# Optimization experiments

Hardware: AMD Instinct MI355X
Metric: run time of the kernel (lower is better)

## Reference

```python
import jax, jax.numpy as jnp
import numpy as np
from jax import lax

B, S, H = 2, 1024, 1024
I = 512            # moe_intermediate_size
E = 32             # n_routed_experts
TOP_K = 4
N_GROUP = 4
TOPK_GROUP = 2
SCALE = 2.5        # routed_scaling_factor
N_SHARED = 2
SH_I = I * N_SHARED


def setup_inputs() -> dict:
    key = jax.random.key(0)
    ks = jax.random.split(key, 10)
    std = 0.02
    return {
        "hidden_states": jax.random.normal(ks[0], (B, S, H), jnp.float32),
        "router_weight": jax.random.normal(ks[1], (E, H), jnp.float32) * std,
        "router_bias": jnp.zeros((E,), jnp.float32),
        "gate_w": jax.random.normal(ks[2], (E, I, H), jnp.float32) * std,
        "up_w": jax.random.normal(ks[3], (E, I, H), jnp.float32) * std,
        "down_w": jax.random.normal(ks[4], (E, H, I), jnp.float32) * std,
        "shared_gate_w": jax.random.normal(ks[5], (SH_I, H), jnp.float32) * std,
        "shared_up_w": jax.random.normal(ks[6], (SH_I, H), jnp.float32) * std,
        "shared_down_w": jax.random.normal(ks[7], (H, SH_I), jnp.float32) * std,
    }


def _route(tokens, router_weight, router_bias):
    # tokens: [T, H] -> topk_idx [T, K] int, topk_weight [T, K] f32
    logits = tokens.astype(jnp.float32) @ router_weight.astype(jnp.float32).T  # [T, E]
    scores = jax.nn.sigmoid(logits)
    sfc = scores + router_bias[None, :]
    T = tokens.shape[0]
    # group scores: sum of top-2 per group
    grp = sfc.reshape(T, N_GROUP, E // N_GROUP)
    group_scores = lax.top_k(grp, 2)[0].sum(-1)                 # [T, n_group]
    _, gidx = lax.top_k(group_scores, TOPK_GROUP)               # [T, topk_group]
    gmask = jax.nn.one_hot(gidx, N_GROUP, dtype=sfc.dtype).sum(1)  # [T, n_group]
    smask = jnp.broadcast_to(gmask[:, :, None], (T, N_GROUP, E // N_GROUP)).reshape(T, E)
    tmp = jnp.where(smask > 0, sfc, 0.0)
    _, topk_idx = lax.top_k(tmp, TOP_K)                         # [T, K]
    topk_w = jnp.take_along_axis(scores, topk_idx, axis=1)
    topk_w = topk_w / (topk_w.sum(-1, keepdims=True) + 1e-20)   # norm_topk_prob
    topk_w = topk_w * SCALE
    return topk_idx, topk_w


def reference(hidden_states, router_weight, router_bias, gate_w, up_w, down_w,
              shared_gate_w, shared_up_w, shared_down_w):
    tokens = hidden_states.reshape(-1, H)                       # [T, H]
    topk_idx, topk_w = _route(tokens, router_weight, router_bias)
    # dense all-expert SwiGLU
    gate_vals = jax.nn.silu(jnp.einsum('th,eih->tei', tokens, gate_w))
    up_vals = jnp.einsum('th,eih->tei', tokens, up_w)
    hidden_vals = gate_vals * up_vals                           # [T, E, I]
    expert_out = jnp.einsum('tei,ehi->teh', hidden_vals, down_w)  # [T, E, H]
    sel = jnp.take_along_axis(expert_out, topk_idx[:, :, None], axis=1)  # [T, K, H]
    mixed = (sel * topk_w[:, :, None].astype(sel.dtype)).sum(1)
    mixed = mixed.reshape(hidden_states.shape)
    # shared experts (dense SwiGLU MLP)
    sg = jax.nn.silu(jnp.einsum('bsh,ih->bsi', hidden_states, shared_gate_w))
    su = jnp.einsum('bsh,ih->bsi', hidden_states, shared_up_w)
    shared = jnp.einsum('bsi,hi->bsh', sg * su, shared_down_w)
    return mixed + shared
```

## Files before the change

### kernel.cpp

```cpp
#include <hip/hip_runtime.h>
#include <hip/hip_bf16.h>
#include <math.h>

#define HD 1024
#define ID 512
#define NE 32
#define NT 2048
#define NG 4
#define SHI 1024
#define SCALE 2.5f

#define BM 128
#define BN 64
#define BK 32
#define LDA 40

typedef __bf16 bf16_t;
typedef __attribute__((ext_vector_type(8))) __bf16 bf16x8;
typedef __attribute__((ext_vector_type(4))) __bf16 bf16x4;
typedef __attribute__((ext_vector_type(4))) float f32x4;

#define LTOK 8
#define LKC 64
__global__ void __launch_bounds__(256) logits_kernel(
    const float* __restrict__ hs, const float* __restrict__ rw,
    float* __restrict__ logits, int* __restrict__ counts)
{
    if (blockIdx.x == 0 && threadIdx.x < NE) counts[threadIdx.x] = 0;

    __shared__ float Xs[LTOK][68];
    __shared__ float Ws[NE][65];

    int tid = threadIdx.x;
    int t0 = blockIdx.x * LTOK;
    int tslot = tid >> 5, ecol = tid & 31;
    float acc = 0.f;

    for (int k0 = 0; k0 < HD; k0 += LKC) {
        if (tid < 128) {
            int row = tid >> 4, q = tid & 15;
            float4 v = *(const float4*)(hs + (size_t)(t0 + row) * HD + k0 + q * 4);
            *(float4*)(&Xs[row][q * 4]) = v;
        }
        #pragma unroll
        for (int i = 0; i < 8; ++i) {
            int idx = i * 256 + tid;
            int e = idx >> 6, kk = idx & 63;
            Ws[e][kk] = rw[(size_t)e * HD + k0 + kk];
        }
        __syncthreads();
        #pragma unroll 8
        for (int kk = 0; kk < LKC; ++kk)
            acc += Xs[tslot][kk] * Ws[ecol][kk];
        __syncthreads();
    }
    logits[(size_t)(t0 + tslot) * NE + ecol] = acc;
}

__global__ void __launch_bounds__(256) topk_kernel(
    const float* __restrict__ logits, const float* __restrict__ rb,
    float* __restrict__ topkw, int* __restrict__ counts, int* __restrict__ lists)
{
    int t = blockIdx.x * 256 + threadIdx.x;
    if (t >= NT) return;

    float scores[NE], sfc[NE], tmp[NE];
    #pragma unroll
    for (int e = 0; e < NE; ++e) {
        float l = logits[(size_t)t * NE + e];
        float s = 1.f / (1.f + __expf(-l));
        scores[e] = s;
        sfc[e] = s + rb[e];
    }
    float gs[NG];
    #pragma unroll
    for (int g = 0; g < NG; ++g) {
        float m1 = -1e30f, m2 = -1e30f;
        #pragma unroll
        for (int j = 0; j < 8; ++j) {
            float v = sfc[g * 8 + j];
            if (v > m1) { m2 = m1; m1 = v; } else if (v > m2) m2 = v;
        }
        gs[g] = m1 + m2;
    }
    int g1 = 0;
    #pragma unroll
    for (int g = 1; g < NG; ++g) if (gs[g] > gs[g1]) g1 = g;
    int g2 = -1;
    #pragma unroll
    for (int g = 0; g < NG; ++g) {
        if (g == g1) continue;
        if (g2 < 0 || gs[g] > gs[g2]) g2 = g;
    }
    #pragma unroll
    for (int e = 0; e < NE; ++e) {
        int g = e >> 3;
        tmp[e] = (g == g1 || g == g2) ? sfc[e] : 0.0f;
    }
    int idx[4]; float wk[4]; float wsum = 0.f;
    #pragma unroll
    for (int k = 0; k < 4; ++k) {
        int best = 0; float bv = -1e30f;
        #pragma unroll
        for (int e = 0; e < NE; ++e) if (tmp[e] > bv) { bv = tmp[e]; best = e; }
        idx[k] = best; tmp[best] = -1e30f;
        wk[k] = scores[best]; wsum += wk[k];
    }
    float inv = SCALE / (wsum + 1e-20f);
    #pragma unroll
    for (int k = 0; k < 4; ++k) {
        int p = t * 4 + k;
        topkw[p] = wk[k] * inv;
        int e = idx[k];
        int pos = atomicAdd(&counts[e], 1);
        lists[e * NT + pos] = p;
    }
}

__device__ inline bf16x4 cvt4(float4 v) {
    bf16x4 r;
    r[0] = (__bf16)v.x; r[1] = (__bf16)v.y; r[2] = (__bf16)v.z; r[3] = (__bf16)v.w;
    return r;
}

template<bool EXPERT, int ND>
__global__ void __launch_bounds__(256) gateup_mfma(
    const float* __restrict__ X, const float* __restrict__ Wg,
    const float* __restrict__ Wu, bf16_t* __restrict__ Hout,
    const int* __restrict__ lists, const int* __restrict__ counts)
{
    int e = 0, cnt = NT;
    const float* wg = Wg; const float* wu = Wu;
    if (EXPERT) {
        e = blockIdx.x; cnt = counts[e];
        wg = Wg + (size_t)e * ND * HD;
        wu = Wu + (size_t)e * ND * HD;
    }
    int mtb = blockIdx.y, ntb = blockIdx.z;
    if (mtb * BM >= cnt) return;

    __shared__ __align__(16) bf16_t As[BM * LDA];
    __shared__ __align__(16) bf16_t Bgs[BN * LDA];
    __shared__ __align__(16) bf16_t Bus[BN * LDA];
    __shared__ int rowid[BM];

    int tid = threadIdx.x;
    if (tid < BM) {
        int gm = mtb * BM + tid;
        int mm = gm < cnt ? gm : cnt - 1;
        rowid[tid] = EXPERT ? lists[e * NT + mm] : mm;
    }
    __syncthreads();

    int lane = tid & 63;
    int w = tid >> 6;
    int wm = w & 1, wn = w >> 1;
    int lrow = lane & 15, quad = lane >> 4;

    f32x4 accg[4][2], accu[4][2];
    #pragma unroll
    for (int i = 0; i < 4; ++i)
        #pragma unroll
        for (int j = 0; j < 2; ++j) { accg[i][j] = (f32x4){0,0,0,0}; accu[i][j] = (f32x4){0,0,0,0}; }

    for (int k0 = 0; k0 < HD; k0 += BK) {
        #pragma unroll
        for (int r = 0; r < (BM * (BK / 4)) / 256; ++r) {
            int idx = r * 256 + tid;
            int row = idx >> 3, kq = idx & 7;
            int tok = EXPERT ? (rowid[row] >> 2) : rowid[row];
            float4 v = *(const float4*)(X + (size_t)tok * HD + k0 + kq * 4);
            *(bf16x4*)(As + row * LDA + kq * 4) = cvt4(v);
        }
        #pragma unroll
        for (int r = 0; r < (BN * (BK / 4)) / 256; ++r) {
            int idx = r * 256 + tid;
            int n = idx >> 3, kq = idx & 7;
            size_t off = (size_t)(ntb * BN + n) * HD + k0 + kq * 4;
            *(bf16x4*)(Bgs + n * LDA + kq * 4) = cvt4(*(const float4*)(wg + off));
            *(bf16x4*)(Bus + n * LDA + kq * 4) = cvt4(*(const float4*)(wu + off));
        }
        __syncthreads();

        bf16x8 af[4], bg[2], bu[2];
        #pragma unroll
        for (int mt = 0; mt < 4; ++mt)
            af[mt] = *(const bf16x8*)(As + (wm * 64 + mt * 16 + lrow) * LDA + quad * 8);
        #pragma unroll
        for (int nt = 0; nt < 2; ++nt) {
            bg[nt] = *(const bf16x8*)(Bgs + (wn * 32 + nt * 16 + lrow) * LDA + quad * 8);
            bu[nt] = *(const bf16x8*)(Bus + (wn * 32 + nt * 16 + lrow) * LDA + quad * 8);
        }
        #pragma unroll
        for (int mt = 0; mt < 4; ++mt)
            #pragma unroll
            for (int nt = 0; nt < 2; ++nt) {
                accg[mt][nt] = __builtin_amdgcn_mfma_f32_16x16x32_bf16(af[mt], bg[nt], accg[mt][nt], 0, 0, 0);
                accu[mt][nt] = __builtin_amdgcn_mfma_f32_16x16x32_bf16(af[mt], bu[nt], accu[mt][nt], 0, 0, 0);
            }
        __syncthreads();
    }

    #pragma unroll
    for (int mt = 0; mt < 4; ++mt)
        #pragma unroll
        for (int r = 0; r < 4; ++r) {
            int row_local = wm * 64 + mt * 16 + quad * 4 + r;
            int gm = mtb * BM + row_local;
            if (gm >= cnt) continue;
            int p = rowid[row_local];
            #pragma unroll
            for (int nt = 0; nt < 2; ++nt) {
                int col = ntb * BN + wn * 32 + nt * 16 + lrow;
                float g = accg[mt][nt][r], u = accu[mt][nt][r];
                float h = (g / (1.f + __expf(-g))) * u;
                Hout[(size_t)p * ND + col] = (__bf16)h;
            }
        }
}

template<bool EXPERT, int KD>
__global__ void __launch_bounds__(256) down_mfma(
    const bf16_t* __restrict__ Hin, const float* __restrict__ Wd,
    float* __restrict__ out, const int* __restrict__ lists,
    const int* __restrict__ counts, const float* __restrict__ topkw)
{
    int e = 0, cnt = NT;
    const float* wd = Wd;
    if (EXPERT) {
        e = blockIdx.x; cnt = counts[e];
        wd = Wd + (size_t)e * HD * KD;
    }
    int mtb = blockIdx.y, ntb = blockIdx.z;
    if (mtb * BM >= cnt) return;

    __shared__ __align__(16) bf16_t As[BM * LDA];
    __shared__ __align__(16) bf16_t Ws[BN * LDA];
    __shared__ int rowid[BM];

    int tid = threadIdx.x;
    if (tid < BM) {
        int gm = mtb * BM + tid;
        int mm = gm < cnt ? gm : cnt - 1;
        rowid[tid] = EXPERT ? lists[e * NT + mm] : mm;
    }
    __syncthreads();

    int lane = tid & 63;
    int w = tid >> 6;
    int wm = w & 1, wn = w >> 1;
    int lrow = lane & 15, quad = lane >> 4;

    f32x4 acc[4][2];
    #pragma unroll
    for (int i = 0; i < 4; ++i)
        #pragma unroll
        for (int j = 0; j < 2; ++j) acc[i][j] = (f32x4){0,0,0,0};

    for (int k0 = 0; k0 < KD; k0 += BK) {
        #pragma unroll
        for (int r = 0; r < (BM * (BK / 8)) / 256; ++r) {
            int idx = r * 256 + tid;
            int row = idx >> 2, c = idx & 3;
            int rp = rowid[row];
            bf16x8 v = *(const bf16x8*)(Hin + (size_t)rp * KD + k0 + c * 8);
            *(bf16x8*)(As + row * LDA + c * 8) = v;
        }
        #pragma unroll
        for (int r = 0; r < (BN * (BK / 4)) / 256; ++r) {
            int idx = r * 256 + tid;
            int n = idx >> 3, kq = idx & 7;
            size_t off = (size_t)(ntb * BN + n) * KD + k0 + kq * 4;
            *(bf16x4*)(Ws + n * LDA + kq * 4) = cvt4(*(const float4*)(wd + off));
        }
        __syncthreads();

        bf16x8 af[4], bf[2];
        #pragma unroll
        for (int mt = 0; mt < 4; ++mt)
            af[mt] = *(const bf16x8*)(As + (wm * 64 + mt * 16 + lrow) * LDA + quad * 8);
        #pragma unroll
        for (int nt = 0; nt < 2; ++nt)
            bf[nt] = *(const bf16x8*)(Ws + (wn * 32 + nt * 16 + lrow) * LDA + quad * 8);
        #pragma unroll
        for (int mt = 0; mt < 4; ++mt)
            #pragma unroll
            for (int nt = 0; nt < 2; ++nt)
                acc[mt][nt] = __builtin_amdgcn_mfma_f32_16x16x32_bf16(af[mt], bf[nt], acc[mt][nt], 0, 0, 0);
        __syncthreads();
    }

    #pragma unroll
    for (int mt = 0; mt < 4; ++mt)
        #pragma unroll
        for (int r = 0; r < 4; ++r) {
            int row_local = wm * 64 + mt * 16 + quad * 4 + r;
            int gm = mtb * BM + row_local;
            if (gm >= cnt) continue;
            int p = rowid[row_local];
            #pragma unroll
            for (int nt = 0; nt < 2; ++nt) {
                int col = ntb * BN + wn * 32 + nt * 16 + lrow;
                float val = acc[mt][nt][r];
                if (EXPERT) {
                    float wgt = topkw[p];
                    atomicAdd(&out[(size_t)(p >> 2) * HD + col], wgt * val);
                } else {
                    out[(size_t)p * HD + col] = val;
                }
            }
        }
}

extern "C" void kernel_launch(void* const* d_in, const int* in_sizes, int n_in,
                              void* d_out, int out_size, void* d_ws, size_t ws_size,
                              hipStream_t stream) {
    const float* hs  = (const float*)d_in[0];
    const float* rw  = (const float*)d_in[1];
    const float* rb  = (const float*)d_in[2];
    const float* gw  = (const float*)d_in[3];
    const float* uw  = (const float*)d_in[4];
    const float* dw  = (const float*)d_in[5];
    const float* sgw = (const float*)d_in[6];
    const float* suw = (const float*)d_in[7];
    const float* sdw = (const float*)d_in[8];
    float* out = (float*)d_out;

    char* ws = (char*)d_ws;
    int*    counts = (int*)ws;
    float*  topkw  = (float*)(ws + 128);
    int*    lists  = (int*)(ws + 128 + 32768);
    float*  logits = (float*)(ws + 128 + 32768 + 262144);
    bf16_t* hbuf   = (bf16_t*)(ws + 128 + 32768 + 262144 + 262144);

    logits_kernel<<<NT / LTOK, 256, 0, stream>>>(hs, rw, logits, counts);
    topk_kernel<<<NT / 256, 256, 0, stream>>>(logits, rb, topkw, counts, lists);

    gateup_mfma<false, SHI><<<dim3(1, NT / BM, SHI / BN), 256, 0, stream>>>(
        hs, sgw, suw, hbuf, nullptr, nullptr);
    down_mfma<false, SHI><<<dim3(1, NT / BM, HD / BN), 256, 0, stream>>>(
        hbuf, sdw, out, nullptr, nullptr, nullptr);

    gateup_mfma<true, ID><<<dim3(NE, NT / BM, ID / BN), 256, 0, stream>>>(
        hs, gw, uw, hbuf, lists, counts);
    down_mfma<true, ID><<<dim3(NE, NT / BM, HD / BN), 256, 0, stream>>>(
        hbuf, dw, out, lists, counts, topkw);
}
```

Before: 418.4 us.

## Prefetch next K-tile into registers and shrink shared-expert M tile

The gate/up and down MFMA kernels now load the next K-slice of activations and weights into registers while the current slice is being multiplied. This overlaps global load latency with compute. The M tile becomes a template parameter, set to 64 for the dense shared-expert GEMMs to launch more blocks and to 128 for the routed experts. The cost is more live registers per thread, which may lower occupancy.

```diff
diff --git a/kernel.cpp b/kernel.cpp
--- a/kernel.cpp
+++ b/kernel.cpp
@@ -10,7 +10,6 @@
 #define SHI 1024
 #define SCALE 2.5f
 
-#define BM 128
 #define BN 64
 #define BK 32
 #define LDA 40
@@ -123,7 +122,7 @@
     return r;
 }
 
-template<bool EXPERT, int ND>
+template<bool EXPERT, int ND, int BMT>
 __global__ void __launch_bounds__(256) gateup_mfma(
     const float* __restrict__ X, const float* __restrict__ Wg,
     const float* __restrict__ Wu, bf16_t* __restrict__ Hout,
@@ -137,62 +136,100 @@
         wu = Wu + (size_t)e * ND * HD;
     }
     int mtb = blockIdx.y, ntb = blockIdx.z;
-    if (mtb * BM >= cnt) return;
-
-    __shared__ __align__(16) bf16_t As[BM * LDA];
+    if (mtb * BMT >= cnt) return;
+
+    __shared__ __align__(16) bf16_t As[BMT * LDA];
     __shared__ __align__(16) bf16_t Bgs[BN * LDA];
     __shared__ __align__(16) bf16_t Bus[BN * LDA];
-    __shared__ int rowid[BM];
+    __shared__ int rowid[BMT];
 
     int tid = threadIdx.x;
-    if (tid < BM) {
-        int gm = mtb * BM + tid;
+    if (tid < BMT) {
+        int gm = mtb * BMT + tid;
         int mm = gm < cnt ? gm : cnt - 1;
         rowid[tid] = EXPERT ? lists[e * NT + mm] : mm;
     }
     __syncthreads();
+
+    constexpr int AR = (BMT * BK) / (256 * 4);
+    constexpr int BR = (BN * BK) / (256 * 4);
+    constexpr int MT = BMT / 32;
 
     int lane = tid & 63;
     int w = tid >> 6;
     int wm = w & 1, wn = w >> 1;
     int lrow = lane & 15, quad = lane >> 4;
 
-    f32x4 accg[4][2], accu[4][2];
-    #pragma unroll
-    for (int i = 0; i < 4; ++i)
+    f32x4 accg[MT][2], accu[MT][2];
+    #pragma unroll
+    for (int i = 0; i < MT; ++i)
         #pragma unroll
         for (int j = 0; j < 2; ++j) { accg[i][j] = (f32x4){0,0,0,0}; accu[i][j] = (f32x4){0,0,0,0}; }
 
+    float4 pa[AR], pbg[BR], pbu[BR];
+
+    #pragma unroll
+    for (int r = 0; r < AR; ++r) {
+        int idx = r * 256 + tid;
+        int row = idx >> 3, kq = idx & 7;
+        int tok = EXPERT ? (rowid[row] >> 2) : rowid[row];
+        pa[r] = *(const float4*)(X + (size_t)tok * HD + kq * 4);
+    }
+    #pragma unroll
+    for (int r = 0; r < BR; ++r) {
+        int idx = r * 256 + tid;
+        int n = idx >> 3, kq = idx & 7;
+        size_t off = (size_t)(ntb * BN + n) * HD + kq * 4;
+        pbg[r] = *(const float4*)(wg + off);
+        pbu[r] = *(const float4*)(wu + off);
+    }
+
     for (int k0 = 0; k0 < HD; k0 += BK) {
         #pragma unroll
-        for (int r = 0; r < (BM * (BK / 4)) / 256; ++r) {
+        for (int r = 0; r < AR; ++r) {
             int idx = r * 256 + tid;
             int row = idx >> 3, kq = idx & 7;
-            int tok = EXPERT ? (rowid[row] >> 2) : rowid[row];
-            float4 v = *(const float4*)(X + (size_t)tok * HD + k0 + kq * 4);
-            *(bf16x4*)(As + row * LDA + kq * 4) = cvt4(v);
-        }
-        #pragma unroll
-        for (int r = 0; r < (BN * (BK / 4)) / 256; ++r) {
+            *(bf16x4*)(As + row * LDA + kq * 4) = cvt4(pa[r]);
+        }
+        #pragma unroll
+        for (int r = 0; r < BR; ++r) {
             int idx = r * 256 + tid;
             int n = idx >> 3, kq = idx & 7;
-            size_t off = (size_t)(ntb * BN + n) * HD + k0 + kq * 4;
-            *(bf16x4*)(Bgs + n * LDA + kq * 4) = cvt4(*(const float4*)(wg + off));
-            *(bf16x4*)(Bus + n * LDA + kq * 4) = cvt4(*(const float4*)(wu + off));
-        }
-        __syncthreads();
-
-        bf16x8 af[4], bg[2], bu[2];
-        #pragma unroll
-        for (int mt = 0; mt < 4; ++mt)
-            af[mt] = *(const bf16x8*)(As + (wm * 64 + mt * 16 + lrow) * LDA + quad * 8);
+            *(bf16x4*)(Bgs + n * LDA + kq * 4) = cvt4(pbg[r]);
+            *(bf16x4*)(Bus + n * LDA + kq * 4) = cvt4(pbu[r]);
+        }
+        __syncthreads();
+
+        int k1 = k0 + BK;
+        if (k1 < HD) {
+            #pragma unroll
+            for (int r = 0; r < AR; ++r) {
+                int idx = r * 256 + tid;
+                int row = idx >> 3, kq = idx & 7;
+                int tok = EXPERT ? (rowid[row] >> 2) : rowid[row];
+                pa[r] = *(const float4*)(X + (size_t)tok * HD + k1 + kq * 4);
+            }
+            #pragma unroll
+            for (int r = 0; r < BR; ++r) {
+                int idx = r * 256 + tid;
+                int n = idx >> 3, kq = idx & 7;
+                size_t off = (size_t)(ntb * BN + n) * HD + k1 + kq * 4;
+                pbg[r] = *(const float4*)(wg + off);
+                pbu[r] = *(const float4*)(wu + off);
+            }
+        }
+
+        bf16x8 af[MT], bg[2], bu[2];
+        #pragma unroll
+        for (int mt = 0; mt < MT; ++mt)
+            af[mt] = *(const bf16x8*)(As + (wm * (BMT / 2) + mt * 16 + lrow) * LDA + quad * 8);
         #pragma unroll
         for (int nt = 0; nt < 2; ++nt) {
             bg[nt] = *(const bf16x8*)(Bgs + (wn * 32 + nt * 16 + lrow) * LDA + quad * 8);
             bu[nt] = *(const bf16x8*)(Bus + (wn * 32 + nt * 16 + lrow) * LDA + quad * 8);
         }
         #pragma unroll
-        for (int mt = 0; mt < 4; ++mt)
+        for (int mt = 0; mt < MT; ++mt)
             #pragma unroll
             for (int nt = 0; nt < 2; ++nt) {
                 accg[mt][nt] = __builtin_amdgcn_mfma_f32_16x16x32_bf16(af[mt], bg[nt], accg[mt][nt], 0, 0, 0);
@@ -202,11 +239,11 @@
     }
 
     #pragma unroll
-    for (int mt = 0; mt < 4; ++mt)
+    for (int mt = 0; mt < MT; ++mt)
         #pragma unroll
         for (int r = 0; r < 4; ++r) {
-            int row_local = wm * 64 + mt * 16 + quad * 4 + r;
-            int gm = mtb * BM + row_local;
+            int row_local = wm * (BMT / 2) + mt * 16 + quad * 4 + r;
+            int gm = mtb * BMT + row_local;
             if (gm >= cnt) continue;
             int p = rowid[row_local];
             #pragma unroll
@@ -219,7 +256,7 @@
         }
 }
 
-template<bool EXPERT, int KD>
+template<bool EXPERT, int KD, int BMT>
 __global__ void __launch_bounds__(256) down_mfma(
     const bf16_t* __restrict__ Hin, const float* __restrict__ Wd,
     float* __restrict__ out, const int* __restrict__ lists,
@@ -232,58 +269,91 @@
         wd = Wd + (size_t)e * HD * KD;
     }
     int mtb = blockIdx.y, ntb = blockIdx.z;
-    if (mtb * BM >= cnt) return;
-
-    __shared__ __align__(16) bf16_t As[BM * LDA];
+    if (mtb * BMT >= cnt) return;
+
+    __shared__ __align__(16) bf16_t As[BMT * LDA];
     __shared__ __align__(16) bf16_t Ws[BN * LDA];
-    __shared__ int rowid[BM];
+    __shared__ int rowid[BMT];
 
     int tid = threadIdx.x;
-    if (tid < BM) {
-        int gm = mtb * BM + tid;
+    if (tid < BMT) {
+        int gm = mtb * BMT + tid;
         int mm = gm < cnt ? gm : cnt - 1;
         rowid[tid] = EXPERT ? lists[e * NT + mm] : mm;
     }
     __syncthreads();
+
+    constexpr int ARH = (BMT * BK / 8) / 256;
+    constexpr int BR = (BN * BK) / (256 * 4);
+    constexpr int MT = BMT / 32;
 
     int lane = tid & 63;
     int w = tid >> 6;
     int wm = w & 1, wn = w >> 1;
     int lrow = lane & 15, quad = lane >> 4;
 
-    f32x4 acc[4][2];
-    #pragma unroll
-    for (int i = 0; i < 4; ++i)
+    f32x4 acc[MT][2];
+    #pragma unroll
+    for (int i = 0; i < MT; ++i)
         #pragma unroll
         for (int j = 0; j < 2; ++j) acc[i][j] = (f32x4){0,0,0,0};
 
+    bf16x8 pa[ARH];
+    float4 pw[BR];
+
+    #pragma unroll
+    for (int r = 0; r < ARH; ++r) {
+        int idx = r * 256 + tid;
+        int row = idx >> 2, c = idx & 3;
+        pa[r] = *(const bf16x8*)(Hin + (size_t)rowid[row] * KD + c * 8);
+    }
+    #pragma unroll
+    for (int r = 0; r < BR; ++r) {
+        int idx = r * 256 + tid;
+        int n = idx >> 3, kq = idx & 7;
+        pw[r] = *(const float4*)(wd + (size_t)(ntb * BN + n) * KD + kq * 4);
+    }
+
     for (int k0 = 0; k0 < KD; k0 += BK) {
         #pragma unroll
-        for (int r = 0; r < (BM * (BK / 8)) / 256; ++r) {
+        for (int r = 0; r < ARH; ++r) {
             int idx = r * 256 + tid;
             int row = idx >> 2, c = idx & 3;
-            int rp = rowid[row];
-            bf16x8 v = *(const bf16x8*)(Hin + (size_t)rp * KD + k0 + c * 8);
-            *(bf16x8*)(As + row * LDA + c * 8) = v;
-        }
-        #pragma unroll
-        for (int r = 0; r < (BN * (BK / 4)) / 256; ++r) {
+            *(bf16x8*)(As + row * LDA + c * 8) = pa[r];
+        }
+        #pragma unroll
+        for (int r = 0; r < BR; ++r) {
             int idx = r * 256 + tid;
             int n = idx >> 3, kq = idx & 7;
-            size_t off = (size_t)(ntb * BN + n) * KD + k0 + kq * 4;
-            *(bf16x4*)(Ws + n * LDA + kq * 4) = cvt4(*(const float4*)(wd + off));
-        }
-        __syncthreads();
-
-        bf16x8 af[4], bf[2];
-        #pragma unroll
-        for (int mt = 0; mt < 4; ++mt)
-            af[mt] = *(const bf16x8*)(As + (wm * 64 + mt * 16 + lrow) * LDA + quad * 8);
+            *(bf16x4*)(Ws + n * LDA + kq * 4) = cvt4(pw[r]);
+        }
+        __syncthreads();
+
+        int k1 = k0 + BK;
+        if (k1 < KD) {
+            #pragma unroll
+            for (int r = 0; r < ARH; ++r) {
+                int idx = r * 256 + tid;
+                int row = idx >> 2, c = idx & 3;
+                pa[r] = *(const bf16x8*)(Hin + (size_t)rowid[row] * KD + k1 + c * 8);
+            }
+            #pragma unroll
+            for (int r = 0; r < BR; ++r) {
+                int idx = r * 256 + tid;
+                int n = idx >> 3, kq = idx & 7;
+                pw[r] = *(const float4*)(wd + (size_t)(ntb * BN + n) * KD + k1 + kq * 4);
+            }
+        }
+
+        bf16x8 af[MT], bf[2];
+        #pragma unroll
+        for (int mt = 0; mt < MT; ++mt)
+            af[mt] = *(const bf16x8*)(As + (wm * (BMT / 2) + mt * 16 + lrow) * LDA + quad * 8);
         #pragma unroll
         for (int nt = 0; nt < 2; ++nt)
             bf[nt] = *(const bf16x8*)(Ws + (wn * 32 + nt * 16 + lrow) * LDA + quad * 8);
         #pragma unroll
-        for (int mt = 0; mt < 4; ++mt)
+        for (int mt = 0; mt < MT; ++mt)
             #pragma unroll
             for (int nt = 0; nt < 2; ++nt)
                 acc[mt][nt] = __builtin_amdgcn_mfma_f32_16x16x32_bf16(af[mt], bf[nt], acc[mt][nt], 0, 0, 0);
@@ -291,11 +361,11 @@
     }
 
     #pragma unroll
-    for (int mt = 0; mt < 4; ++mt)
+    for (int mt = 0; mt < MT; ++mt)
         #pragma unroll
         for (int r = 0; r < 4; ++r) {
-            int row_local = wm * 64 + mt * 16 + quad * 4 + r;
-            int gm = mtb * BM + row_local;
+            int row_local = wm * (BMT / 2) + mt * 16 + quad * 4 + r;
+            int gm = mtb * BMT + row_local;
             if (gm >= cnt) continue;
             int p = rowid[row_local];
             #pragma unroll
@@ -336,13 +406,13 @@
     logits_kernel<<<NT / LTOK, 256, 0, stream>>>(hs, rw, logits, counts);
     topk_kernel<<<NT / 256, 256, 0, stream>>>(logits, rb, topkw, counts, lists);
 
-    gateup_mfma<false, SHI><<<dim3(1, NT / BM, SHI / BN), 256, 0, stream>>>(
+    gateup_mfma<false, SHI, 64><<<dim3(1, NT / 64, SHI / BN), 256, 0, stream>>>(
         hs, sgw, suw, hbuf, nullptr, nullptr);
-    down_mfma<false, SHI><<<dim3(1, NT / BM, HD / BN), 256, 0, stream>>>(
+    down_mfma<false, SHI, 64><<<dim3(1, NT / 64, HD / BN), 256, 0, stream>>>(
         hbuf, sdw, out, nullptr, nullptr, nullptr);
 
-    gateup_mfma<true, ID><<<dim3(NE, NT / BM, ID / BN), 256, 0, stream>>>(
+    gateup_mfma<true, ID, 128><<<dim3(NE, NT / 128, ID / BN), 256, 0, stream>>>(
         hs, gw, uw, hbuf, lists, counts);
-    down_mfma<true, ID><<<dim3(NE, NT / BM, HD / BN), 256, 0, stream>>>(
+    down_mfma<true, ID, 128><<<dim3(NE, NT / 128, HD / BN), 256, 0, stream>>>(
         hbuf, dw, out, lists, counts, topkw);
 }
```

New measurement: 411.6 us. About the same (-1.6%).

## Pre-convert inputs and weights to bf16, stage tiles via global_load_lds

Applied to the files above, without the earlier changes.

Adds a conversion pass that writes bf16 copies of hidden states and all expert and shared weights into the workspace. New GEMM kernels then load tiles straight into LDS with global_load_lds, dropping per-tile fp32 loads and register-side conversion. The old fp32 path is kept as a fallback when the workspace is too small. The trade-off is an extra full read and write of every weight on each call (about 200MB of fp32 read), plus unpadded LDS layouts that may cause bank conflicts.

```diff
diff --git a/kernel.cpp b/kernel.cpp
--- a/kernel.cpp
+++ b/kernel.cpp
@@ -10,15 +10,33 @@
 #define SHI 1024
 #define SCALE 2.5f
 
-#define BM 128
-#define BN 64
 #define BK 32
-#define LDA 40
+#define LDAF 40
 
 typedef __bf16 bf16_t;
 typedef __attribute__((ext_vector_type(8))) __bf16 bf16x8;
 typedef __attribute__((ext_vector_type(4))) __bf16 bf16x4;
 typedef __attribute__((ext_vector_type(4))) float f32x4;
+
+__device__ inline void load_lds16(const void* g, void* l) {
+    __builtin_amdgcn_global_load_lds(
+        (const __attribute__((address_space(1))) void*)g,
+        (__attribute__((address_space(3))) void*)l, 16, 0, 0);
+}
+
+__global__ void __launch_bounds__(256) cvt_bf16_kernel(
+    const float* __restrict__ in, bf16_t* __restrict__ out, int n8)
+{
+    int stride = gridDim.x * 256;
+    for (int i = blockIdx.x * 256 + threadIdx.x; i < n8; i += stride) {
+        const float4* p = (const float4*)(in + (size_t)i * 8);
+        float4 a = p[0], b = p[1];
+        bf16x8 v;
+        v[0] = (__bf16)a.x; v[1] = (__bf16)a.y; v[2] = (__bf16)a.z; v[3] = (__bf16)a.w;
+        v[4] = (__bf16)b.x; v[5] = (__bf16)b.y; v[6] = (__bf16)b.z; v[7] = (__bf16)b.w;
+        *(bf16x8*)(out + (size_t)i * 8) = v;
+    }
+}
 
 #define LTOK 8
 #define LKC 64
@@ -123,8 +141,200 @@
     return r;
 }
 
+
 template<bool EXPERT, int ND>
-__global__ void __launch_bounds__(256) gateup_mfma(
+__global__ void __launch_bounds__(256) gateup_bf16(
+    const bf16_t* __restrict__ X, const bf16_t* __restrict__ Wg,
+    const bf16_t* __restrict__ Wu, bf16_t* __restrict__ Hout,
+    const int* __restrict__ lists, const int* __restrict__ counts)
+{
+    int e = 0, cnt = NT;
+    const bf16_t* wg = Wg; const bf16_t* wu = Wu;
+    if (EXPERT) {
+        e = blockIdx.x; cnt = counts[e];
+        wg = Wg + (size_t)e * ND * HD;
+        wu = Wu + (size_t)e * ND * HD;
+    }
+    int mtb = blockIdx.y, ntb = blockIdx.z;
+    if (mtb * 128 >= cnt) return;
+
+    __shared__ __align__(16) bf16_t As[128 * 32];
+    __shared__ __align__(16) bf16_t Bgs[64 * 32];
+    __shared__ __align__(16) bf16_t Bus[64 * 32];
+    __shared__ int rowid[128];
+
+    int tid = threadIdx.x;
+    if (tid < 128) {
+        int gm = mtb * 128 + tid;
+        int mm = gm < cnt ? gm : cnt - 1;
+        rowid[tid] = EXPERT ? lists[e * NT + mm] : mm;
+    }
+    __syncthreads();
+
+    int lane = tid & 63, w = tid >> 6;
+    int wm = w & 1, wn = w >> 1;
+    int lrow = lane & 15, quad = lane >> 4;
+
+    int sr = lane >> 2, sc = lane & 3;
+    int arow0 = w * 32 + sr;
+    int arow1 = w * 32 + 16 + sr;
+    int tokA0 = EXPERT ? (rowid[arow0] >> 2) : rowid[arow0];
+    int tokA1 = EXPERT ? (rowid[arow1] >> 2) : rowid[arow1];
+    const bf16_t* ga0 = X + (size_t)tokA0 * HD + sc * 8;
+    const bf16_t* ga1 = X + (size_t)tokA1 * HD + sc * 8;
+    bf16_t* la0 = As + (w * 32) * 32 + lane * 8;
+    bf16_t* la1 = As + (w * 32 + 16) * 32 + lane * 8;
+
+    int brow = w * 16 + sr;
+    const bf16_t* gbg = wg + (size_t)(ntb * 64 + brow) * HD + sc * 8;
+    const bf16_t* gbu = wu + (size_t)(ntb * 64 + brow) * HD + sc * 8;
+    bf16_t* lbg = Bgs + (w * 16) * 32 + lane * 8;
+    bf16_t* lbu = Bus + (w * 16) * 32 + lane * 8;
+
+    f32x4 accg[4][2], accu[4][2];
+    #pragma unroll
+    for (int i = 0; i < 4; ++i)
+        #pragma unroll
+        for (int j = 0; j < 2; ++j) { accg[i][j] = (f32x4){0,0,0,0}; accu[i][j] = (f32x4){0,0,0,0}; }
+
+    for (int k0 = 0; k0 < HD; k0 += BK) {
+        load_lds16(ga0 + k0, la0);
+        load_lds16(ga1 + k0, la1);
+        load_lds16(gbg + k0, lbg);
+        load_lds16(gbu + k0, lbu);
+        __syncthreads();
+
+        bf16x8 af[4], bg[2], bu[2];
+        #pragma unroll
+        for (int mt = 0; mt < 4; ++mt)
+            af[mt] = *(const bf16x8*)(As + (wm * 64 + mt * 16 + lrow) * 32 + quad * 8);
+        #pragma unroll
+        for (int nt = 0; nt < 2; ++nt) {
+            bg[nt] = *(const bf16x8*)(Bgs + (wn * 32 + nt * 16 + lrow) * 32 + quad * 8);
+            bu[nt] = *(const bf16x8*)(Bus + (wn * 32 + nt * 16 + lrow) * 32 + quad * 8);
+        }
+        #pragma unroll
+        for (int mt = 0; mt < 4; ++mt)
+            #pragma unroll
+            for (int nt = 0; nt < 2; ++nt) {
+                accg[mt][nt] = __builtin_amdgcn_mfma_f32_16x16x32_bf16(af[mt], bg[nt], accg[mt][nt], 0, 0, 0);
+                accu[mt][nt] = __builtin_amdgcn_mfma_f32_16x16x32_bf16(af[mt], bu[nt], accu[mt][nt], 0, 0, 0);
+            }
+        __syncthreads();
+    }
+
+    #pragma unroll
+    for (int mt = 0; mt < 4; ++mt)
+        #pragma unroll
+        for (int r = 0; r < 4; ++r) {
+            int row_local = wm * 64 + mt * 16 + quad * 4 + r;
+            int gm = mtb * 128 + row_local;
+            if (gm >= cnt) continue;
+            int p = rowid[row_local];
+            #pragma unroll
+            for (int nt = 0; nt < 2; ++nt) {
+                int col = ntb * 64 + wn * 32 + nt * 16 + lrow;
+                float g = accg[mt][nt][r], u = accu[mt][nt][r];
+                float h = (g / (1.f + __expf(-g))) * u;
+                Hout[(size_t)p * ND + col] = (__bf16)h;
+            }
+        }
+}
+
+template<bool EXPERT, int KD>
+__global__ void __launch_bounds__(256) down_bf16(
+    const bf16_t* __restrict__ Hin, const bf16_t* __restrict__ Wd,
+    float* __restrict__ out, const int* __restrict__ lists,
+    const int* __restrict__ counts, const float* __restrict__ topkw)
+{
+    int e = 0, cnt = NT;
+    const bf16_t* wd = Wd;
+    if (EXPERT) {
+        e = blockIdx.x; cnt = counts[e];
+        wd = Wd + (size_t)e * HD * KD;
+    }
+    int mtb = blockIdx.y, ntb = blockIdx.z;
+    if (mtb * 128 >= cnt) return;
+
+    __shared__ __align__(16) bf16_t As[128 * 32];
+    __shared__ __align__(16) bf16_t Bs[64 * 32];
+    __shared__ int rowid[128];
+
+    int tid = threadIdx.x;
+    if (tid < 128) {
+        int gm = mtb * 128 + tid;
+        int mm = gm < cnt ? gm : cnt - 1;
+        rowid[tid] = EXPERT ? lists[e * NT + mm] : mm;
+    }
+    __syncthreads();
+
+    int lane = tid & 63, w = tid >> 6;
+    int wm = w & 1, wn = w >> 1;
+    int lrow = lane & 15, quad = lane >> 4;
+
+    int sr = lane >> 2, sc = lane & 3;
+    int arow0 = w * 32 + sr;
+    int arow1 = w * 32 + 16 + sr;
+    const bf16_t* ga0 = Hin + (size_t)rowid[arow0] * KD + sc * 8;
+    const bf16_t* ga1 = Hin + (size_t)rowid[arow1] * KD + sc * 8;
+    bf16_t* la0 = As + (w * 32) * 32 + lane * 8;
+    bf16_t* la1 = As + (w * 32 + 16) * 32 + lane * 8;
+
+    int brow = w * 16 + sr;
+    const bf16_t* gb = wd + (size_t)(ntb * 64 + brow) * KD + sc * 8;
+    bf16_t* lb = Bs + (w * 16) * 32 + lane * 8;
+
+    f32x4 acc[4][2];
+    #pragma unroll
+    for (int i = 0; i < 4; ++i)
+        #pragma unroll
+        for (int j = 0; j < 2; ++j) acc[i][j] = (f32x4){0,0,0,0};
+
+    for (int k0 = 0; k0 < KD; k0 += BK) {
+        load_lds16(ga0 + k0, la0);
+        load_lds16(ga1 + k0, la1);
+        load_lds16(gb + k0, lb);
+        __syncthreads();
+
+        bf16x8 af[4], bf[2];
+        #pragma unroll
+        for (int mt = 0; mt < 4; ++mt)
+            af[mt] = *(const bf16x8*)(As + (wm * 64 + mt * 16 + lrow) * 32 + quad * 8);
+        #pragma unroll
+        for (int nt = 0; nt < 2; ++nt)
+            bf[nt] = *(const bf16x8*)(Bs + (wn * 32 + nt * 16 + lrow) * 32 + quad * 8);
+        #pragma unroll
+        for (int mt = 0; mt < 4; ++mt)
+            #pragma unroll
+            for (int nt = 0; nt < 2; ++nt)
+                acc[mt][nt] = __builtin_amdgcn_mfma_f32_16x16x32_bf16(af[mt], bf[nt], acc[mt][nt], 0, 0, 0);
+        __syncthreads();
+    }
+
+    #pragma unroll
+    for (int mt = 0; mt < 4; ++mt)
+        #pragma unroll
+        for (int r = 0; r < 4; ++r) {
+            int row_local = wm * 64 + mt * 16 + quad * 4 + r;
+            int gm = mtb * 128 + row_local;
+            if (gm >= cnt) continue;
+            int p = rowid[row_local];
+            #pragma unroll
+            for (int nt = 0; nt < 2; ++nt) {
+                int col = ntb * 64 + wn * 32 + nt * 16 + lrow;
+                float val = acc[mt][nt][r];
+                if (EXPERT) {
+                    float wgt = topkw[p];
+                    atomicAdd(&out[(size_t)(p >> 2) * HD + col], wgt * val);
+                } else {
+                    out[(size_t)p * HD + col] = val;
+                }
+            }
+        }
+}
+
+template<bool EXPERT, int ND>
+__global__ void __launch_bounds__(256) gateup_f32(
     const float* __restrict__ X, const float* __restrict__ Wg,
     const float* __restrict__ Wu, bf16_t* __restrict__ Hout,
     const int* __restrict__ lists, const int* __restrict__ counts)
@@ -137,23 +347,22 @@
         wu = Wu + (size_t)e * ND * HD;
     }
     int mtb = blockIdx.y, ntb = blockIdx.z;
-    if (mtb * BM >= cnt) return;
-
-    __shared__ __align__(16) bf16_t As[BM * LDA];
-    __shared__ __align__(16) bf16_t Bgs[BN * LDA];
-    __shared__ __align__(16) bf16_t Bus[BN * LDA];
-    __shared__ int rowid[BM];
+    if (mtb * 128 >= cnt) return;
+
+    __shared__ __align__(16) bf16_t As[128 * LDAF];
+    __shared__ __align__(16) bf16_t Bgs[64 * LDAF];
+    __shared__ __align__(16) bf16_t Bus[64 * LDAF];
+    __shared__ int rowid[128];
 
     int tid = threadIdx.x;
-    if (tid < BM) {
-        int gm = mtb * BM + tid;
+    if (tid < 128) {
+        int gm = mtb * 128 + tid;
         int mm = gm < cnt ? gm : cnt - 1;
         rowid[tid] = EXPERT ? lists[e * NT + mm] : mm;
     }
     __syncthreads();
 
-    int lane = tid & 63;
-    int w = tid >> 6;
+    int lane = tid & 63, w = tid >> 6;
     int wm = w & 1, wn = w >> 1;
     int lrow = lane & 15, quad = lane >> 4;
 
@@ -165,31 +374,31 @@
 
     for (int k0 = 0; k0 < HD; k0 += BK) {
         #pragma unroll
-        for (int r = 0; r < (BM * (BK / 4)) / 256; ++r) {
+        for (int r = 0; r < 4; ++r) {
             int idx = r * 256 + tid;
             int row = idx >> 3, kq = idx & 7;
             int tok = EXPERT ? (rowid[row] >> 2) : rowid[row];
             float4 v = *(const float4*)(X + (size_t)tok * HD + k0 + kq * 4);
-            *(bf16x4*)(As + row * LDA + kq * 4) = cvt4(v);
-        }
-        #pragma unroll
-        for (int r = 0; r < (BN * (BK / 4)) / 256; ++r) {
+            *(bf16x4*)(As + row * LDAF + kq * 4) = cvt4(v);
+        }
+        #pragma unroll
+        for (int r = 0; r < 2; ++r) {
             int idx = r * 256 + tid;
             int n = idx >> 3, kq = idx & 7;
-            size_t off = (size_t)(ntb * BN + n) * HD + k0 + kq * 4;
-            *(bf16x4*)(Bgs + n * LDA + kq * 4) = cvt4(*(const float4*)(wg + off));
-            *(bf16x4*)(Bus + n * LDA + kq * 4) = cvt4(*(const float4*)(wu + off));
+            size_t off = (size_t)(ntb * 64 + n) * HD + k0 + kq * 4;
+            *(bf16x4*)(Bgs + n * LDAF + kq * 4) = cvt4(*(const float4*)(wg + off));
+            *(bf16x4*)(Bus + n * LDAF + kq * 4) = cvt4(*(const float4*)(wu + off));
         }
         __syncthreads();
 
         bf16x8 af[4], bg[2], bu[2];
         #pragma unroll
         for (int mt = 0; mt < 4; ++mt)
-            af[mt] = *(const bf16x8*)(As + (wm * 64 + mt * 16 + lrow) * LDA + quad * 8);
+            af[mt] = *(const bf16x8*)(As + (wm * 64 + mt * 16 + lrow) * LDAF + quad * 8);
         #pragma unroll
         for (int nt = 0; nt < 2; ++nt) {
-            bg[nt] = *(const bf16x8*)(Bgs + (wn * 32 + nt * 16 + lrow) * LDA + quad * 8);
-            bu[nt] = *(const bf16x8*)(Bus + (wn * 32 + nt * 16 + lrow) * LDA + quad * 8);
+            bg[nt] = *(const bf16x8*)(Bgs + (wn * 32 + nt * 16 + lrow) * LDAF + quad * 8);
+            bu[nt] = *(const bf16x8*)(Bus + (wn * 32 + nt * 16 + lrow) * LDAF + quad * 8);
         }
         #pragma unroll
         for (int mt = 0; mt < 4; ++mt)
@@ -206,12 +415,12 @@
         #pragma unroll
         for (int r = 0; r < 4; ++r) {
             int row_local = wm * 64 + mt * 16 + quad * 4 + r;
-            int gm = mtb * BM + row_local;
+            int gm = mtb * 128 + row_local;
             if (gm >= cnt) continue;
             int p = rowid[row_local];
             #pragma unroll
             for (int nt = 0; nt < 2; ++nt) {
-                int col = ntb * BN + wn * 32 + nt * 16 + lrow;
+                int col = ntb * 64 + wn * 32 + nt * 16 + lrow;
                 float g = accg[mt][nt][r], u = accu[mt][nt][r];
                 float h = (g / (1.f + __expf(-g))) * u;
                 Hout[(size_t)p * ND + col] = (__bf16)h;
@@ -220,7 +429,7 @@
 }
 
 template<bool EXPERT, int KD>
-__global__ void __launch_bounds__(256) down_mfma(
+__global__ void __launch_bounds__(256) down_f32(
     const bf16_t* __restrict__ Hin, const float* __restrict__ Wd,
     float* __restrict__ out, const int* __restrict__ lists,
     const int* __restrict__ counts, const float* __restrict__ topkw)
@@ -232,22 +441,21 @@
         wd = Wd + (size_t)e * HD * KD;
     }
     int mtb = blockIdx.y, ntb = blockIdx.z;
-    if (mtb * BM >= cnt) return;
-
-    __shared__ __align__(16) bf16_t As[BM * LDA];
-    __shared__ __align__(16) bf16_t Ws[BN * LDA];
-    __shared__ int rowid[BM];
+    if (mtb * 128 >= cnt) return;
+
+    __shared__ __align__(16) bf16_t As[128 * LDAF];
+    __shared__ __align__(16) bf16_t Bs[64 * LDAF];
+    __shared__ int rowid[128];
 
     int tid = threadIdx.x;
-    if (tid < BM) {
-        int gm = mtb * BM + tid;
+    if (tid < 128) {
+        int gm = mtb * 128 + tid;
         int mm = gm < cnt ? gm : cnt - 1;
         rowid[tid] = EXPERT ? lists[e * NT + mm] : mm;
     }
     __syncthreads();
 
-    int lane = tid & 63;
-    int w = tid >> 6;
+    int lane = tid & 63, w = tid >> 6;
     int wm = w & 1, wn = w >> 1;
     int lrow = lane & 15, quad = lane >> 4;
 
@@ -259,29 +467,28 @@
 
     for (int k0 = 0; k0 < KD; k0 += BK) {
         #pragma unroll
-        for (int r = 0; r < (BM * (BK / 8)) / 256; ++r) {
+        for (int r = 0; r < 2; ++r) {
             int idx = r * 256 + tid;
             int row = idx >> 2, c = idx & 3;
-            int rp = rowid[row];
-            bf16x8 v = *(const bf16x8*)(Hin + (size_t)rp * KD + k0 + c * 8);
-            *(bf16x8*)(As + row * LDA + c * 8) = v;
-        }
-        #pragma unroll
-        for (int r = 0; r < (BN * (BK / 4)) / 256; ++r) {
+            bf16x8 v = *(const bf16x8*)(Hin + (size_t)rowid[row] * KD + k0 + c * 8);
+            *(bf16x8*)(As + row * LDAF + c * 8) = v;
+        }
+        #pragma unroll
+        for (int r = 0; r < 2; ++r) {
             int idx = r * 256 + tid;
             int n = idx >> 3, kq = idx & 7;
-            size_t off = (size_t)(ntb * BN + n) * KD + k0 + kq * 4;
-            *(bf16x4*)(Ws + n * LDA + kq * 4) = cvt4(*(const float4*)(wd + off));
+            size_t off = (size_t)(ntb * 64 + n) * KD + k0 + kq * 4;
+            *(bf16x4*)(Bs + n * LDAF + kq * 4) = cvt4(*(const float4*)(wd + off));
         }
         __syncthreads();
 
         bf16x8 af[4], bf[2];
         #pragma unroll
         for (int mt = 0; mt < 4; ++mt)
-            af[mt] = *(const bf16x8*)(As + (wm * 64 + mt * 16 + lrow) * LDA + quad * 8);
+            af[mt] = *(const bf16x8*)(As + (wm * 64 + mt * 16 + lrow) * LDAF + quad * 8);
         #pragma unroll
         for (int nt = 0; nt < 2; ++nt)
-            bf[nt] = *(const bf16x8*)(Ws + (wn * 32 + nt * 16 + lrow) * LDA + quad * 8);
+            bf[nt] = *(const bf16x8*)(Bs + (wn * 32 + nt * 16 + lrow) * LDAF + quad * 8);
         #pragma unroll
         for (int mt = 0; mt < 4; ++mt)
             #pragma unroll
@@ -295,12 +502,12 @@
         #pragma unroll
         for (int r = 0; r < 4; ++r) {
             int row_local = wm * 64 + mt * 16 + quad * 4 + r;
-            int gm = mtb * BM + row_local;
+            int gm = mtb * 128 + row_local;
             if (gm >= cnt) continue;
             int p = rowid[row_local];
             #pragma unroll
             for (int nt = 0; nt < 2; ++nt) {
-                int col = ntb * BN + wn * 32 + nt * 16 + lrow;
+                int col = ntb * 64 + wn * 32 + nt * 16 + lrow;
                 float val = acc[mt][nt][r];
                 if (EXPERT) {
                     float wgt = topkw[p];
@@ -327,22 +534,52 @@
     float* out = (float*)d_out;
 
     char* ws = (char*)d_ws;
-    int*    counts = (int*)ws;
-    float*  topkw  = (float*)(ws + 128);
-    int*    lists  = (int*)(ws + 128 + 32768);
-    float*  logits = (float*)(ws + 128 + 32768 + 262144);
-    bf16_t* hbuf   = (bf16_t*)(ws + 128 + 32768 + 262144 + 262144);
+    size_t off = 0;
+    int*    counts = (int*)(ws + off);   off += 128;
+    float*  topkw  = (float*)(ws + off); off += (size_t)NT * 4 * 4;
+    int*    lists  = (int*)(ws + off);   off += (size_t)NE * NT * 4;
+    float*  logits = (float*)(ws + off); off += (size_t)NT * NE * 4;
+    bf16_t* hbuf   = (bf16_t*)(ws + off); off += (size_t)NT * 4 * ID * 2;
+    size_t base_small = off;
+    bf16_t* hsb  = (bf16_t*)(ws + off); off += (size_t)NT * HD * 2;
+    bf16_t* gwb  = (bf16_t*)(ws + off); off += (size_t)NE * ID * HD * 2;
+    bf16_t* uwb  = (bf16_t*)(ws + off); off += (size_t)NE * ID * HD * 2;
+    bf16_t* dwb  = (bf16_t*)(ws + off); off += (size_t)NE * HD * ID * 2;
+    bf16_t* sgwb = (bf16_t*)(ws + off); off += (size_t)SHI * HD * 2;
+    bf16_t* suwb = (bf16_t*)(ws + off); off += (size_t)SHI * HD * 2;
+    bf16_t* sdwb = (bf16_t*)(ws + off); off += (size_t)HD * SHI * 2;
+    bool big = (ws_size >= off);
+    (void)base_small;
 
     logits_kernel<<<NT / LTOK, 256, 0, stream>>>(hs, rw, logits, counts);
     topk_kernel<<<NT / 256, 256, 0, stream>>>(logits, rb, topkw, counts, lists);
 
-    gateup_mfma<false, SHI><<<dim3(1, NT / BM, SHI / BN), 256, 0, stream>>>(
-        hs, sgw, suw, hbuf, nullptr, nullptr);
-    down_mfma<false, SHI><<<dim3(1, NT / BM, HD / BN), 256, 0, stream>>>(
-        hbuf, sdw, out, nullptr, nullptr, nullptr);
-
-    gateup_mfma<true, ID><<<dim3(NE, NT / BM, ID / BN), 256, 0, stream>>>(
-        hs, gw, uw, hbuf, lists, counts);
-    down_mfma<true, ID><<<dim3(NE, NT / BM, HD / BN), 256, 0, stream>>>(
-        hbuf, dw, out, lists, counts, topkw);
-}
+    if (big) {
+        cvt_bf16_kernel<<<512, 256, 0, stream>>>(hs, hsb, NT * HD / 8);
+        cvt_bf16_kernel<<<2048, 256, 0, stream>>>(gw, gwb, NE * ID * HD / 8);
+        cvt_bf16_kernel<<<2048, 256, 0, stream>>>(uw, uwb, NE * ID * HD / 8);
+        cvt_bf16_kernel<<<2048, 256, 0, stream>>>(dw, dwb, NE * HD * ID / 8);
+        cvt_bf16_kernel<<<512, 256, 0, stream>>>(sgw, sgwb, SHI * HD / 8);
+        cvt_bf16_kernel<<<512, 256, 0, stream>>>(suw, suwb, SHI * HD / 8);
+        cvt_bf16_kernel<<<512, 256, 0, stream>>>(sdw, sdwb, HD * SHI / 8);
+
+        gateup_bf16<false, SHI><<<dim3(1, NT / 128, SHI / 64), 256, 0, stream>>>(
+            hsb, sgwb, suwb, hbuf, nullptr, nullptr);
+        down_bf16<false, SHI><<<dim3(1, NT / 128, HD / 64), 256, 0, stream>>>(
+            hbuf, sdwb, out, nullptr, nullptr, nullptr);
+
+        gateup_bf16<true, ID><<<dim3(NE, NT / 128, ID / 64), 256, 0, stream>>>(
+            hsb, gwb, uwb, hbuf, lists, counts);
+        down_bf16<true, ID><<<dim3(NE, NT / 128, HD / 64), 256, 0, stream>>>(
+            hbuf, dwb, out, lists, counts, topkw);
+    } else {
+        gateup_f32<false, SHI><<<dim3(1, NT / 128, SHI / 64), 256, 0, stream>>>(
+            hs, sgw, suw, hbuf, nullptr, nullptr);
+        down_f32<false, SHI><<<dim3(1, NT / 128, HD / 64), 256, 0, stream>>>(
+            hbuf, sdw, out, nullptr, nullptr, nullptr);
+        gateup_f32<true, ID><<<dim3(NE, NT / 128, ID / 64), 256, 0, stream>>>(
+            hs, gw, uw, hbuf, lists, counts);
+        down_f32<true, ID><<<dim3(NE, NT / 128, HD / 64), 256, 0, stream>>>(
+            hbuf, dw, out, lists, counts, topkw);
+    }
+}
```

Result: no change. 416.0 us (-0.6%).
